# Kernel optimization log

Hardware: AMD Instinct MI355X
Metric: run time of the kernel (lower is better)

The kernel has to match this reference:

```python
import jax, jax.numpy as jnp
import numpy as np

WS = 7       # window size per spatial dim
SHIFT = 3    # cyclic shift = WS // 2
HEADS = 6


def _rel_pos_index():
    # [N, N] index into the (2*WS-1)^3 relative-position-bias table
    c = np.stack(np.meshgrid(np.arange(WS), np.arange(WS), np.arange(WS), indexing='ij')).reshape(3, -1)
    rel = (c[:, :, None] - c[:, None, :]).transpose(1, 2, 0) + (WS - 1)
    rel[:, :, 0] *= (2 * WS - 1) ** 2
    rel[:, :, 1] *= (2 * WS - 1)
    return rel.sum(-1)


def _attn_mask(D, H, W):
    # shifted-window attention mask: [nW, N, N] with 0 / -100
    img = np.zeros((D, H, W))
    sl = (slice(0, -WS), slice(-WS, -SHIFT), slice(-SHIFT, None))
    cnt = 0
    for d in sl:
        for h in sl:
            for w in sl:
                img[d, h, w] = cnt
                cnt += 1
    m = img.reshape(D // WS, WS, H // WS, WS, W // WS, WS).transpose(0, 2, 4, 1, 3, 5).reshape(-1, WS ** 3)
    return np.where(m[:, None, :] != m[:, :, None], -100.0, 0.0).astype(np.float32)


def _ln(x, g, b):
    mu = x.mean(-1, keepdims=True)
    var = ((x - mu) ** 2).mean(-1, keepdims=True)
    return (x - mu) * jax.lax.rsqrt(var + 1e-5) * g + b


def _win_part(x):
    B, D, H, W, C = x.shape
    x = x.reshape(B, D // WS, WS, H // WS, WS, W // WS, WS, C)
    return x.transpose(0, 1, 3, 5, 2, 4, 6, 7).reshape(B, -1, WS ** 3, C)


def _win_rev(xw, D, H, W):
    B, _, _, C = xw.shape
    x = xw.reshape(B, D // WS, H // WS, W // WS, WS, WS, WS, C)
    return x.transpose(0, 1, 4, 2, 5, 3, 6, 7).reshape(B, D, H, W, C)


def setup_inputs() -> dict:
    key = jax.random.key(0)
    ks = jax.random.split(key, 8)
    C, dff, Nh = 192, 768, HEADS
    s = 0.02
    return {
        'x': jax.random.normal(ks[0], (2, 28, 28, 28, C), jnp.float32),
        'ln1_g': jnp.ones((C,), jnp.float32),
        'ln1_b': jnp.zeros((C,), jnp.float32),
        'qkv_w': jax.random.normal(ks[1], (3 * C, C), jnp.float32) * s,
        'qkv_b': jnp.zeros((3 * C,), jnp.float32),
        'rpb': jax.random.normal(ks[2], ((2 * WS - 1) ** 3, Nh), jnp.float32) * s,
        'proj_w': jax.random.normal(ks[3], (C, C), jnp.float32) * s,
        'proj_b': jnp.zeros((C,), jnp.float32),
        'ln2_g': jnp.ones((C,), jnp.float32),
        'ln2_b': jnp.zeros((C,), jnp.float32),
        'fc1_w': jax.random.normal(ks[4], (dff, C), jnp.float32) * s,
        'fc1_b': jnp.zeros((dff,), jnp.float32),
        'fc2_w': jax.random.normal(ks[5], (C, dff), jnp.float32) * s,
        'fc2_b': jnp.zeros((C,), jnp.float32),
    }


def reference(x, ln1_g, ln1_b, qkv_w, qkv_b, rpb, proj_w, proj_b, ln2_g, ln2_b, fc1_w, fc1_b, fc2_w, fc2_b):
    B, D, H, W, C = x.shape
    hd = C // HEADS
    N = WS ** 3
    idx = jnp.asarray(_rel_pos_index())          # [N, N] int
    mask = jnp.asarray(_attn_mask(D, H, W))      # [nW, N, N]

    shortcut = x
    h = _ln(x, ln1_g, ln1_b)
    h = jnp.roll(h, (-SHIFT, -SHIFT, -SHIFT), axis=(1, 2, 3))
    xw = _win_part(h)                            # [B, nW, N, C]
    nW = xw.shape[1]

    qkv = xw @ qkv_w.T + qkv_b                   # [B, nW, N, 3C]
    qkv = qkv.reshape(B, nW, N, 3, HEADS, hd).transpose(3, 0, 1, 4, 2, 5)  # [3,B,nW,h,N,hd]
    q, k, v = qkv[0], qkv[1], qkv[2]

    scale = hd ** -0.5
    attn = jnp.einsum('bwhnd,bwhmd->bwhnm', q * scale, k)  # [B,nW,h,N,N]
    bias = rpb[idx].transpose(2, 0, 1)           # [h, N, N]
    attn = attn + bias + mask[None, :, None]
    attn = jax.nn.softmax(attn, axis=-1)

    o = jnp.einsum('bwhnm,bwhmd->bwhnd', attn, v)
    o = o.transpose(0, 1, 3, 2, 4).reshape(B, nW, N, C)
    o = o @ proj_w.T + proj_b
    o = _win_rev(o, D, H, W)
    o = jnp.roll(o, (SHIFT, SHIFT, SHIFT), axis=(1, 2, 3))

    x = shortcut + o
    h2 = _ln(x, ln2_g, ln2_b)
    h2 = jax.nn.gelu(h2 @ fc1_w.T + fc1_b, approximate=False)
    return x + (h2 @ fc2_w.T + fc2_b)
```

## Files before the change

### kernel.cpp

```cpp
#include <hip/hip_runtime.h>
#include <hip/hip_bf16.h>
#include <math.h>

typedef __hip_bfloat16 bf16;
typedef unsigned short u16;
typedef __attribute__((ext_vector_type(8))) short bf16x8;
typedef __attribute__((ext_vector_type(4))) short bf16x4;
typedef __attribute__((ext_vector_type(4))) float f32x4;

__device__ __forceinline__ float us2f(u16 u) { return __uint_as_float(((unsigned)u) << 16); }
__device__ __forceinline__ u16 f2us(float f) { bf16 h = __float2bfloat16(f); return *(u16*)&h; }

__device__ __forceinline__ float wave_bcast_sum(float v) {
#pragma unroll
    for (int off = 32; off > 0; off >>= 1) v += __shfl_down(v, off);
    return __shfl(v, 0);
}

__device__ __forceinline__ void glds16(const u16* g, u16* l) {
    __builtin_amdgcn_global_load_lds((const __attribute__((address_space(1))) void*)g,
                                     (__attribute__((address_space(3))) void*)l, 16, 0, 0);
}

__global__ __launch_bounds__(256) void k_f2b(const float* __restrict__ in, u16* __restrict__ out, int n) {
    int i = blockIdx.x * 256 + threadIdx.x;
    if (i < n) out[i] = f2us(in[i]);
}

__global__ __launch_bounds__(256) void k_bias(const float* __restrict__ rpb, float* __restrict__ bt) {
    int idx = blockIdx.x * 256 + threadIdx.x;
    if (idx >= 6 * 343 * 352) return;
    int h = idx / (343 * 352);
    int r = idx - h * (343 * 352);
    int n = r / 352, m = r - n * 352;
    float v = 0.0f;
    if (m < 343) {
        int ni = n / 49, nr = n - ni * 49, nj = nr / 7, nk = nr - nj * 7;
        int mi = m / 49, mr = m - mi * 49, mj = mr / 7, mk = mr - mj * 7;
        int d = (ni - mi) * 169 + (nj - mj) * 13 + (nk - mk) + 1098;
        v = rpb[d * 6 + h] * 1.4426950408889634f;
    }
    bt[idx] = v;
}

__global__ __launch_bounds__(256) void k_ln1_winpart(
    const float* __restrict__ x, const float* __restrict__ g, const float* __restrict__ b,
    u16* __restrict__ out)
{
    int lane = threadIdx.x & 63;
    int t = blockIdx.x * 4 + (threadIdx.x >> 6);
    int bidx = t / (64 * 343);
    int r = t - bidx * (64 * 343);
    int w = r / 343;
    int n = r - w * 343;
    int wd = w >> 4, wh = (w >> 2) & 3, ww = w & 3;
    int i = n / 49, rem = n - i * 49;
    int j = rem / 7, k = rem - j * 7;
    int sd = wd * 7 + i + 3; if (sd >= 28) sd -= 28;
    int sh = wh * 7 + j + 3; if (sh >= 28) sh -= 28;
    int sw = ww * 7 + k + 3; if (sw >= 28) sw -= 28;
    size_t src = ((((size_t)bidx * 28 + sd) * 28 + sh) * 28 + sw) * 192;
    float v0 = x[src + lane], v1 = x[src + lane + 64], v2 = x[src + lane + 128];
    float s  = wave_bcast_sum(v0 + v1 + v2);
    float mu = s * (1.0f / 192.0f);
    float s2 = wave_bcast_sum(v0 * v0 + v1 * v1 + v2 * v2);
    float rs = rsqrtf(s2 * (1.0f / 192.0f) - mu * mu + 1e-5f);
    u16* op = out + (size_t)t * 192;
    op[lane]       = f2us((v0 - mu) * rs * g[lane]       + b[lane]);
    op[lane + 64]  = f2us((v1 - mu) * rs * g[lane + 64]  + b[lane + 64]);
    op[lane + 128] = f2us((v2 - mu) * rs * g[lane + 128] + b[lane + 128]);
}

__global__ __launch_bounds__(256) void k_add_winrev_ln2(
    const float* __restrict__ x, const u16* __restrict__ projw,
    const float* __restrict__ g, const float* __restrict__ b,
    float* __restrict__ x1, u16* __restrict__ h2)
{
    int lane = threadIdx.x & 63;
    int t = blockIdx.x * 4 + (threadIdx.x >> 6);
    int sw_ = t % 28, t1 = t / 28;
    int sh_ = t1 % 28, t2 = t1 / 28;
    int sd_ = t2 % 28, bidx = t2 / 28;
    int rd = sd_ + 25; if (rd >= 28) rd -= 28;
    int rh = sh_ + 25; if (rh >= 28) rh -= 28;
    int rw = sw_ + 25; if (rw >= 28) rw -= 28;
    int wd = rd / 7, i = rd - wd * 7;
    int wh = rh / 7, j = rh - wh * 7;
    int ww = rw / 7, k = rw - ww * 7;
    int w = (wd << 4) + (wh << 2) + ww;
    int n = (i * 7 + j) * 7 + k;
    size_t src = (((size_t)(bidx * 64 + w)) * 343 + n) * 192;
    const float* xp = x + (size_t)t * 192;
    float v0 = xp[lane]       + us2f(projw[src + lane]);
    float v1 = xp[lane + 64]  + us2f(projw[src + lane + 64]);
    float v2 = xp[lane + 128] + us2f(projw[src + lane + 128]);
    float* op = x1 + (size_t)t * 192;
    op[lane] = v0; op[lane + 64] = v1; op[lane + 128] = v2;
    float s  = wave_bcast_sum(v0 + v1 + v2);
    float mu = s * (1.0f / 192.0f);
    float s2 = wave_bcast_sum(v0 * v0 + v1 * v1 + v2 * v2);
    float rs = rsqrtf(s2 * (1.0f / 192.0f) - mu * mu + 1e-5f);
    u16* hp = h2 + (size_t)t * 192;
    hp[lane]       = f2us((v0 - mu) * rs * g[lane]       + b[lane]);
    hp[lane + 64]  = f2us((v1 - mu) * rs * g[lane + 64]  + b[lane + 64]);
    hp[lane + 128] = f2us((v2 - mu) * rs * g[lane + 128] + b[lane + 128]);
}

template<int ACT, int OUT>
__global__ __launch_bounds__(256) void k_gemm_mfma(
    const u16* __restrict__ A, const u16* __restrict__ W, const float* __restrict__ bias,
    u16* __restrict__ outB, float* __restrict__ outF, const float* __restrict__ resid,
    int M, int Nc, int K)
{
    __shared__ __align__(16) u16 As[128 * 32];
    __shared__ __align__(16) u16 Bs[64 * 32];
    int tid = threadIdx.x;
    int lane = tid & 63, wv = tid >> 6;
    int quad = lane >> 4, l16 = lane & 15;
    int m0 = blockIdx.y << 7, n0 = blockIdx.x << 6;

    f32x4 acc[2][4] = {};
    int rowA0 = tid >> 2;
    int rowA1 = rowA0 + 64;
    int koff = (tid & 3) << 3;

    const u16* gA0 = A + (size_t)(m0 + rowA0) * K + koff;
    const u16* gA1 = A + (size_t)(m0 + rowA1) * K + koff;
    const u16* gB0 = W + (size_t)(n0 + rowA0) * K + koff;
    u16* lA0 = &As[wv * 512];
    u16* lA1 = &As[2048 + wv * 512];
    u16* lB0 = &Bs[wv * 512];

    for (int k0 = 0; k0 < K; k0 += 32) {
        glds16(gA0 + k0, lA0);
        glds16(gA1 + k0, lA1);
        glds16(gB0 + k0, lB0);
        __syncthreads();
        bf16x8 af[2], bfr[4];
#pragma unroll
        for (int mt = 0; mt < 2; mt++)
            af[mt] = *(const bf16x8*)&As[(wv * 32 + mt * 16 + l16) * 32 + quad * 8];
#pragma unroll
        for (int nt = 0; nt < 4; nt++)
            bfr[nt] = *(const bf16x8*)&Bs[(nt * 16 + l16) * 32 + quad * 8];
#pragma unroll
        for (int mt = 0; mt < 2; mt++)
#pragma unroll
            for (int nt = 0; nt < 4; nt++)
                acc[mt][nt] = __builtin_amdgcn_mfma_f32_16x16x32_bf16(af[mt], bfr[nt], acc[mt][nt], 0, 0, 0);
        __syncthreads();
    }
#pragma unroll
    for (int mt = 0; mt < 2; mt++) {
#pragma unroll
        for (int nt = 0; nt < 4; nt++) {
#pragma unroll
            for (int r = 0; r < 4; r++) {
                int m = m0 + wv * 32 + mt * 16 + quad * 4 + r;
                int n = n0 + nt * 16 + l16;
                float v = acc[mt][nt][r] + bias[n];
                if (ACT == 1) v = 0.5f * v * (1.0f + erff(v * 0.70710678118654752f));
                size_t off = (size_t)m * Nc + n;
                if (OUT == 1) outB[off] = f2us(v);
                else outF[off] = resid[off] + v;
            }
        }
    }
}

__global__ __launch_bounds__(256) void k_attn(
    const u16* __restrict__ qkv, const float* __restrict__ biasT, u16* __restrict__ o_win)
{
    int head = blockIdx.x;
    int w = blockIdx.y;
    int bidx = blockIdx.z;
    __shared__ __align__(16) u16 Ks[352 * 36];
    __shared__ __align__(16) u16 Vt[32 * 352];
    __shared__ __align__(16) u16 Pb[4][16 * 36];
    __shared__ unsigned char lab[352];
    int tid = threadIdx.x;
    int lane = tid & 63, wv = tid >> 6;
    int quad = lane >> 4, l16 = lane & 15;
    size_t base = ((size_t)(bidx * 64 + w)) * 343;

    for (int i = tid; i < 2816; i += 256) {
        int m = i >> 3;
        int d4 = (i & 7) << 2;
        ushort4 kv = {0, 0, 0, 0}, vv = {0, 0, 0, 0};
        if (m < 343) {
            size_t off = (base + m) * 576 + head * 32 + d4;
            kv = *(const ushort4*)(qkv + off + 192);
            vv = *(const ushort4*)(qkv + off + 384);
        }
        *(ushort4*)&Ks[m * 36 + d4] = kv;
        Vt[(d4 + 0) * 352 + m] = vv.x;
        Vt[(d4 + 1) * 352 + m] = vv.y;
        Vt[(d4 + 2) * 352 + m] = vv.z;
        Vt[(d4 + 3) * 352 + m] = vv.w;
    }
    int wd = w >> 4, wh = (w >> 2) & 3, ww = w & 3;
    for (int n = tid; n < 352; n += 256) {
        unsigned char lv = 255;
        if (n < 343) {
            int i = n / 49, rem = n - i * 49;
            int j = rem / 7, k = rem - j * 7;
            int gd = wd * 7 + i, gh = wh * 7 + j, gw = ww * 7 + k;
            int ld_ = (gd < 21) ? 0 : ((gd < 25) ? 1 : 2);
            int lh_ = (gh < 21) ? 0 : ((gh < 25) ? 1 : 2);
            int lw_ = (gw < 21) ? 0 : ((gw < 25) ? 1 : 2);
            lv = (unsigned char)(ld_ * 9 + lh_ * 3 + lw_);
        }
        lab[n] = lv;
    }
    __syncthreads();

    const float SL = 0.17677669529663687f * 1.4426950408889634f;
    u16* pbw = &Pb[wv][0];
    const f32x4 zero = {0.0f, 0.0f, 0.0f, 0.0f};

    for (int rt = wv; rt < 22; rt += 4) {
        int na = rt * 16 + l16; if (na > 342) na = 342;
        bf16x8 af = *(const bf16x8*)(qkv + (base + na) * 576 + head * 32 + quad * 8);
        int lr[4]; const float* bp[4];
#pragma unroll
        for (int r = 0; r < 4; r++) {
            int n = rt * 16 + quad * 4 + r; if (n > 342) n = 342;
            lr[r] = lab[n];
            bp[r] = biasT + ((size_t)(head * 343 + n)) * 352;
        }
        f32x4 o0 = zero, o1 = zero;
        float psum[4] = {0.0f, 0.0f, 0.0f, 0.0f};
        for (int c = 0; c < 11; c++) {
            int m0i = c * 32 + l16;
            int m1i = m0i + 16;
            float b0[4], b1[4];
#pragma unroll
            for (int r = 0; r < 4; r++) { b0[r] = bp[r][m0i]; b1[r] = bp[r][m1i]; }
            int lm0 = lab[m0i], lm1 = lab[m1i];
            const u16* kr0 = &Ks[m0i * 36 + quad * 8];
            const u16* kr1 = &Ks[m1i * 36 + quad * 8];
            bf16x4 k0a = *(const bf16x4*)kr0, k0b = *(const bf16x4*)(kr0 + 4);
            bf16x4 k1a = *(const bf16x4*)kr1, k1b = *(const bf16x4*)(kr1 + 4);
            bf16x8 kb0 = __builtin_shufflevector(k0a, k0b, 0, 1, 2, 3, 4, 5, 6, 7);
            bf16x8 kb1 = __builtin_shufflevector(k1a, k1b, 0, 1, 2, 3, 4, 5, 6, 7);
            f32x4 s0 = __builtin_amdgcn_mfma_f32_16x16x32_bf16(af, kb0, zero, 0, 0, 0);
            f32x4 s1 = __builtin_amdgcn_mfma_f32_16x16x32_bf16(af, kb1, zero, 0, 0, 0);
#pragma unroll
            for (int r = 0; r < 4; r++) {
                float p0 = exp2f(fmaf(s0[r], SL, b0[r]));
                p0 = (lm0 == lr[r]) ? p0 : 0.0f;
                psum[r] += p0;
                pbw[(quad * 4 + r) * 36 + l16] = f2us(p0);
                float p1 = exp2f(fmaf(s1[r], SL, b1[r]));
                p1 = (lm1 == lr[r]) ? p1 : 0.0f;
                psum[r] += p1;
                pbw[(quad * 4 + r) * 36 + 16 + l16] = f2us(p1);
            }
            asm volatile("s_waitcnt lgkmcnt(0)" ::: "memory");
            const u16* pr = &pbw[l16 * 36 + quad * 8];
            bf16x4 pa0 = *(const bf16x4*)pr, pa1 = *(const bf16x4*)(pr + 4);
            bf16x8 pa = __builtin_shufflevector(pa0, pa1, 0, 1, 2, 3, 4, 5, 6, 7);
            bf16x8 vb0 = *(const bf16x8*)&Vt[l16 * 352 + c * 32 + quad * 8];
            bf16x8 vb1 = *(const bf16x8*)&Vt[(16 + l16) * 352 + c * 32 + quad * 8];
            o0 = __builtin_amdgcn_mfma_f32_16x16x32_bf16(pa, vb0, o0, 0, 0, 0);
            o1 = __builtin_amdgcn_mfma_f32_16x16x32_bf16(pa, vb1, o1, 0, 0, 0);
        }
#pragma unroll
        for (int r = 0; r < 4; r++) {
#pragma unroll
            for (int off = 1; off < 16; off <<= 1)
                psum[r] += __shfl_xor(psum[r], off);
        }
#pragma unroll
        for (int r = 0; r < 4; r++) {
            int n = rt * 16 + quad * 4 + r;
            if (n < 343) {
                float inv = 1.0f / psum[r];
                u16* op = o_win + (base + n) * 192 + head * 32;
                op[l16]      = f2us(o0[r] * inv);
                op[l16 + 16] = f2us(o1[r] * inv);
            }
        }
    }
}

extern "C" void kernel_launch(void* const* d_in, const int* in_sizes, int n_in,
                              void* d_out, int out_size, void* d_ws, size_t ws_size,
                              hipStream_t stream)
{
    const float* x      = (const float*)d_in[0];
    const float* ln1_g  = (const float*)d_in[1];
    const float* ln1_b  = (const float*)d_in[2];
    const float* qkv_w  = (const float*)d_in[3];
    const float* qkv_b  = (const float*)d_in[4];
    const float* rpb    = (const float*)d_in[5];
    const float* proj_w = (const float*)d_in[6];
    const float* proj_b = (const float*)d_in[7];
    const float* ln2_g  = (const float*)d_in[8];
    const float* ln2_b  = (const float*)d_in[9];
    const float* fc1_w  = (const float*)d_in[10];
    const float* fc1_b  = (const float*)d_in[11];
    const float* fc2_w  = (const float*)d_in[12];
    const float* fc2_b  = (const float*)d_in[13];

    const int M = 43904;
    const size_t MC  = (size_t)M * 192;
    const size_t MC2 = MC * 2;

    char* ws = (char*)d_ws;
    u16* hA     = (u16*)ws;
    u16* qkvb   = (u16*)(ws + MC2);
    u16* projw  = (u16*)(ws + MC2);
    u16* gbuf   = (u16*)(ws + MC2);
    u16* fc1_wb = (u16*)(ws + 51u * 1024 * 1024);
    u16* fc2_wb = (u16*)(ws + 51u * 1024 * 1024 + 294912);
    float* out  = (float*)d_out;
    u16* qkv_wb  = (u16*)d_out;
    u16* proj_wb = (u16*)d_out + 110592;
    float* biasT = (float*)((char*)d_out + 4u * 1024 * 1024);

    k_f2b<<<432, 256, 0, stream>>>(qkv_w, qkv_wb, 110592);
    k_f2b<<<144, 256, 0, stream>>>(proj_w, proj_wb, 36864);
    k_bias<<<2830, 256, 0, stream>>>(rpb, biasT);
    k_ln1_winpart<<<M / 4, 256, 0, stream>>>(x, ln1_g, ln1_b, hA);
    k_gemm_mfma<0, 1><<<dim3(9, 343), 256, 0, stream>>>(hA, qkv_wb, qkv_b, qkvb, nullptr, nullptr, M, 576, 192);
    k_attn<<<dim3(6, 64, 2), 256, 0, stream>>>(qkvb, biasT, hA);
    k_f2b<<<576, 256, 0, stream>>>(fc1_w, fc1_wb, 147456);
    k_f2b<<<576, 256, 0, stream>>>(fc2_w, fc2_wb, 147456);
    k_gemm_mfma<0, 1><<<dim3(3, 343), 256, 0, stream>>>(hA, proj_wb, proj_b, projw, nullptr, nullptr, M, 192, 192);
    k_add_winrev_ln2<<<M / 4, 256, 0, stream>>>(x, projw, ln2_g, ln2_b, out, hA);
    const int CH0 = 22016, CH1 = 21888;
    k_gemm_mfma<1, 1><<<dim3(12, 172), 256, 0, stream>>>(hA, fc1_wb, fc1_b, gbuf, nullptr, nullptr, CH0, 768, 192);
    k_gemm_mfma<0, 2><<<dim3(3, 172), 256, 0, stream>>>(gbuf, fc2_wb, fc2_b, nullptr, out, out, CH0, 192, 768);
    k_gemm_mfma<1, 1><<<dim3(12, 171), 256, 0, stream>>>(hA + (size_t)CH0 * 192, fc1_wb, fc1_b, gbuf, nullptr, nullptr, CH1, 768, 192);
    k_gemm_mfma<0, 2><<<dim3(3, 171), 256, 0, stream>>>(gbuf, fc2_wb, fc2_b, nullptr, out + (size_t)CH0 * 192, out + (size_t)CH0 * 192, CH1, 192, 768);
}
```

Measured before the change: 340.9 us.

## Rewrite window attention with 32x32 MFMA transposed scores and register-resident P

The attention kernel switches from 16x16x32 to 32x32x16 MFMA tiles. It computes S transposed (keys by queries), so the probabilities can be repacked in registers with v_permlane32_swap and fed straight into the PV MFMA, which removes the per-wave LDS staging buffer for P and its wait. To support this, the bias table is stored transposed and padded to 352x352, and the LDS strides are changed. Separately, the GEMM gains double-buffered LDS so the next K-slice's global-to-LDS load overlaps the current MFMAs. The cost is more LDS in the GEMM and strided bias reads in attention.

```diff
diff --git a/kernel.cpp b/kernel.cpp
--- a/kernel.cpp
+++ b/kernel.cpp
@@ -5,8 +5,9 @@
 typedef __hip_bfloat16 bf16;
 typedef unsigned short u16;
 typedef __attribute__((ext_vector_type(8))) short bf16x8;
-typedef __attribute__((ext_vector_type(4))) short bf16x4;
 typedef __attribute__((ext_vector_type(4))) float f32x4;
+typedef __attribute__((ext_vector_type(16))) float f32x16;
+typedef __attribute__((ext_vector_type(4))) unsigned u32x4;
 
 __device__ __forceinline__ float us2f(u16 u) { return __uint_as_float(((unsigned)u) << 16); }
 __device__ __forceinline__ u16 f2us(float f) { bf16 h = __float2bfloat16(f); return *(u16*)&h; }
@@ -29,12 +30,12 @@
 
 __global__ __launch_bounds__(256) void k_bias(const float* __restrict__ rpb, float* __restrict__ bt) {
     int idx = blockIdx.x * 256 + threadIdx.x;
-    if (idx >= 6 * 343 * 352) return;
-    int h = idx / (343 * 352);
-    int r = idx - h * (343 * 352);
-    int n = r / 352, m = r - n * 352;
+    if (idx >= 6 * 352 * 352) return;
+    int h = idx / (352 * 352);
+    int r = idx - h * (352 * 352);
+    int m = r / 352, n = r - m * 352;
     float v = 0.0f;
-    if (m < 343) {
+    if (m < 343 && n < 343) {
         int ni = n / 49, nr = n - ni * 49, nj = nr / 7, nk = nr - nj * 7;
         int mi = m / 49, mr = m - mi * 49, mj = mr / 7, mk = mr - mj * 7;
         int d = (ni - mi) * 169 + (nj - mj) * 13 + (nk - mk) + 1098;
@@ -112,8 +113,8 @@
     u16* __restrict__ outB, float* __restrict__ outF, const float* __restrict__ resid,
     int M, int Nc, int K)
 {
-    __shared__ __align__(16) u16 As[128 * 32];
-    __shared__ __align__(16) u16 Bs[64 * 32];
+    __shared__ __align__(16) u16 As[2][128 * 32];
+    __shared__ __align__(16) u16 Bs[2][64 * 32];
     int tid = threadIdx.x;
     int lane = tid & 63, wv = tid >> 6;
     int quad = lane >> 4, l16 = lane & 15;
@@ -127,38 +128,47 @@
     const u16* gA0 = A + (size_t)(m0 + rowA0) * K + koff;
     const u16* gA1 = A + (size_t)(m0 + rowA1) * K + koff;
     const u16* gB0 = W + (size_t)(n0 + rowA0) * K + koff;
-    u16* lA0 = &As[wv * 512];
-    u16* lA1 = &As[2048 + wv * 512];
-    u16* lB0 = &Bs[wv * 512];
-
-    for (int k0 = 0; k0 < K; k0 += 32) {
-        glds16(gA0 + k0, lA0);
-        glds16(gA1 + k0, lA1);
-        glds16(gB0 + k0, lB0);
-        __syncthreads();
+
+    int nt = K >> 5;
+    glds16(gA0, &As[0][wv * 512]);
+    glds16(gA1, &As[0][2048 + wv * 512]);
+    glds16(gB0, &Bs[0][wv * 512]);
+    asm volatile("s_waitcnt vmcnt(0)" ::: "memory");
+    __builtin_amdgcn_s_barrier();
+
+    int cur = 0;
+    for (int t = 0; t < nt; ++t) {
+        if (t + 1 < nt) {
+            int k1 = (t + 1) << 5;
+            glds16(gA0 + k1, &As[cur ^ 1][wv * 512]);
+            glds16(gA1 + k1, &As[cur ^ 1][2048 + wv * 512]);
+            glds16(gB0 + k1, &Bs[cur ^ 1][wv * 512]);
+        }
         bf16x8 af[2], bfr[4];
 #pragma unroll
         for (int mt = 0; mt < 2; mt++)
-            af[mt] = *(const bf16x8*)&As[(wv * 32 + mt * 16 + l16) * 32 + quad * 8];
-#pragma unroll
-        for (int nt = 0; nt < 4; nt++)
-            bfr[nt] = *(const bf16x8*)&Bs[(nt * 16 + l16) * 32 + quad * 8];
+            af[mt] = *(const bf16x8*)&As[cur][(wv * 32 + mt * 16 + l16) * 32 + quad * 8];
+#pragma unroll
+        for (int nt2 = 0; nt2 < 4; nt2++)
+            bfr[nt2] = *(const bf16x8*)&Bs[cur][(nt2 * 16 + l16) * 32 + quad * 8];
 #pragma unroll
         for (int mt = 0; mt < 2; mt++)
 #pragma unroll
-            for (int nt = 0; nt < 4; nt++)
-                acc[mt][nt] = __builtin_amdgcn_mfma_f32_16x16x32_bf16(af[mt], bfr[nt], acc[mt][nt], 0, 0, 0);
-        __syncthreads();
+            for (int nt2 = 0; nt2 < 4; nt2++)
+                acc[mt][nt2] = __builtin_amdgcn_mfma_f32_16x16x32_bf16(af[mt], bfr[nt2], acc[mt][nt2], 0, 0, 0);
+        asm volatile("s_waitcnt vmcnt(0)" ::: "memory");
+        __builtin_amdgcn_s_barrier();
+        cur ^= 1;
     }
 #pragma unroll
     for (int mt = 0; mt < 2; mt++) {
 #pragma unroll
-        for (int nt = 0; nt < 4; nt++) {
+        for (int nt2 = 0; nt2 < 4; nt2++) {
 #pragma unroll
             for (int r = 0; r < 4; r++) {
                 int m = m0 + wv * 32 + mt * 16 + quad * 4 + r;
-                int n = n0 + nt * 16 + l16;
-                float v = acc[mt][nt][r] + bias[n];
+                int n = n0 + nt2 * 16 + l16;
+                float v = acc[mt][nt2][r] + bias[n];
                 if (ACT == 1) v = 0.5f * v * (1.0f + erff(v * 0.70710678118654752f));
                 size_t off = (size_t)m * Nc + n;
                 if (OUT == 1) outB[off] = f2us(v);
@@ -174,13 +184,13 @@
     int head = blockIdx.x;
     int w = blockIdx.y;
     int bidx = blockIdx.z;
-    __shared__ __align__(16) u16 Ks[352 * 36];
-    __shared__ __align__(16) u16 Vt[32 * 352];
-    __shared__ __align__(16) u16 Pb[4][16 * 36];
+    __shared__ __align__(16) u16 Ks[352 * 40];
+    __shared__ __align__(16) u16 Vt[32 * 360];
+    __shared__ float invs[4][32];
     __shared__ unsigned char lab[352];
     int tid = threadIdx.x;
     int lane = tid & 63, wv = tid >> 6;
-    int quad = lane >> 4, l16 = lane & 15;
+    int hi = lane >> 5, l31 = lane & 31;
     size_t base = ((size_t)(bidx * 64 + w)) * 343;
 
     for (int i = tid; i < 2816; i += 256) {
@@ -192,11 +202,11 @@
             kv = *(const ushort4*)(qkv + off + 192);
             vv = *(const ushort4*)(qkv + off + 384);
         }
-        *(ushort4*)&Ks[m * 36 + d4] = kv;
-        Vt[(d4 + 0) * 352 + m] = vv.x;
-        Vt[(d4 + 1) * 352 + m] = vv.y;
-        Vt[(d4 + 2) * 352 + m] = vv.z;
-        Vt[(d4 + 3) * 352 + m] = vv.w;
+        *(ushort4*)&Ks[m * 40 + d4] = kv;
+        Vt[(d4 + 0) * 360 + m] = vv.x;
+        Vt[(d4 + 1) * 360 + m] = vv.y;
+        Vt[(d4 + 2) * 360 + m] = vv.z;
+        Vt[(d4 + 3) * 360 + m] = vv.w;
     }
     int wd = w >> 4, wh = (w >> 2) & 3, ww = w & 3;
     for (int n = tid; n < 352; n += 256) {
@@ -215,70 +225,73 @@
     __syncthreads();
 
     const float SL = 0.17677669529663687f * 1.4426950408889634f;
-    u16* pbw = &Pb[wv][0];
-    const f32x4 zero = {0.0f, 0.0f, 0.0f, 0.0f};
-
-    for (int rt = wv; rt < 22; rt += 4) {
-        int na = rt * 16 + l16; if (na > 342) na = 342;
-        bf16x8 af = *(const bf16x8*)(qkv + (base + na) * 576 + head * 32 + quad * 8);
-        int lr[4]; const float* bp[4];
-#pragma unroll
-        for (int r = 0; r < 4; r++) {
-            int n = rt * 16 + quad * 4 + r; if (n > 342) n = 342;
-            lr[r] = lab[n];
-            bp[r] = biasT + ((size_t)(head * 343 + n)) * 352;
-        }
-        f32x4 o0 = zero, o1 = zero;
-        float psum[4] = {0.0f, 0.0f, 0.0f, 0.0f};
-        for (int c = 0; c < 11; c++) {
-            int m0i = c * 32 + l16;
-            int m1i = m0i + 16;
-            float b0[4], b1[4];
-#pragma unroll
-            for (int r = 0; r < 4; r++) { b0[r] = bp[r][m0i]; b1[r] = bp[r][m1i]; }
-            int lm0 = lab[m0i], lm1 = lab[m1i];
-            const u16* kr0 = &Ks[m0i * 36 + quad * 8];
-            const u16* kr1 = &Ks[m1i * 36 + quad * 8];
-            bf16x4 k0a = *(const bf16x4*)kr0, k0b = *(const bf16x4*)(kr0 + 4);
-            bf16x4 k1a = *(const bf16x4*)kr1, k1b = *(const bf16x4*)(kr1 + 4);
-            bf16x8 kb0 = __builtin_shufflevector(k0a, k0b, 0, 1, 2, 3, 4, 5, 6, 7);
-            bf16x8 kb1 = __builtin_shufflevector(k1a, k1b, 0, 1, 2, 3, 4, 5, 6, 7);
-            f32x4 s0 = __builtin_amdgcn_mfma_f32_16x16x32_bf16(af, kb0, zero, 0, 0, 0);
-            f32x4 s1 = __builtin_amdgcn_mfma_f32_16x16x32_bf16(af, kb1, zero, 0, 0, 0);
-#pragma unroll
-            for (int r = 0; r < 4; r++) {
-                float p0 = exp2f(fmaf(s0[r], SL, b0[r]));
-                p0 = (lm0 == lr[r]) ? p0 : 0.0f;
-                psum[r] += p0;
-                pbw[(quad * 4 + r) * 36 + l16] = f2us(p0);
-                float p1 = exp2f(fmaf(s1[r], SL, b1[r]));
-                p1 = (lm1 == lr[r]) ? p1 : 0.0f;
-                psum[r] += p1;
-                pbw[(quad * 4 + r) * 36 + 16 + l16] = f2us(p1);
+    const f32x16 z16 = {0,0,0,0,0,0,0,0,0,0,0,0,0,0,0,0};
+
+    for (int tile = wv; tile < 11; tile += 4) {
+        int n0 = tile * 32;
+        int nq = n0 + l31; if (nq > 342) nq = 342;
+        const u16* qp = qkv + (base + nq) * 576 + head * 32;
+        bf16x8 bq0 = *(const bf16x8*)(qp + hi * 8);
+        bf16x8 bq1 = *(const bf16x8*)(qp + 16 + hi * 8);
+        unsigned lr = lab[n0 + l31];
+        const float* bq = biasT + (size_t)head * 352 * 352 + n0 + l31;
+
+        f32x16 o = z16;
+        float psum = 0.0f;
+        for (int c = 0; c < 11; ++c) {
+            int mb = c * 32;
+            const u16* kp = &Ks[(mb + l31) * 40 + hi * 8];
+            bf16x8 ka0 = *(const bf16x8*)kp;
+            bf16x8 ka1 = *(const bf16x8*)(kp + 16);
+            f32x16 s = __builtin_amdgcn_mfma_f32_32x32x16_bf16(ka0, bq0, z16, 0, 0, 0);
+            s = __builtin_amdgcn_mfma_f32_32x32x16_bf16(ka1, bq1, s, 0, 0, 0);
+            unsigned labw[4];
+#pragma unroll
+            for (int g = 0; g < 4; ++g)
+                labw[g] = *(const unsigned*)&lab[mb + hi * 4 + g * 8];
+            float p[16];
+#pragma unroll
+            for (int r = 0; r < 16; ++r) {
+                int g = r >> 2, q = r & 3;
+                float bb = bq[(size_t)(mb + 4 * hi + 8 * g + q) * 352];
+                float e = exp2f(fmaf(s[r], SL, bb));
+                p[r] = (((labw[g] >> (8 * q)) & 255u) == lr) ? e : 0.0f;
+                psum += p[r];
             }
-            asm volatile("s_waitcnt lgkmcnt(0)" ::: "memory");
-            const u16* pr = &pbw[l16 * 36 + quad * 8];
-            bf16x4 pa0 = *(const bf16x4*)pr, pa1 = *(const bf16x4*)(pr + 4);
-            bf16x8 pa = __builtin_shufflevector(pa0, pa1, 0, 1, 2, 3, 4, 5, 6, 7);
-            bf16x8 vb0 = *(const bf16x8*)&Vt[l16 * 352 + c * 32 + quad * 8];
-            bf16x8 vb1 = *(const bf16x8*)&Vt[(16 + l16) * 352 + c * 32 + quad * 8];
-            o0 = __builtin_amdgcn_mfma_f32_16x16x32_bf16(pa, vb0, o0, 0, 0, 0);
-            o1 = __builtin_amdgcn_mfma_f32_16x16x32_bf16(pa, vb1, o1, 0, 0, 0);
-        }
-#pragma unroll
-        for (int r = 0; r < 4; r++) {
-#pragma unroll
-            for (int off = 1; off < 16; off <<= 1)
-                psum[r] += __shfl_xor(psum[r], off);
-        }
-#pragma unroll
-        for (int r = 0; r < 4; r++) {
-            int n = rt * 16 + quad * 4 + r;
+            unsigned pk0 = (unsigned)f2us(p[0])  | ((unsigned)f2us(p[1])  << 16);
+            unsigned pk1 = (unsigned)f2us(p[2])  | ((unsigned)f2us(p[3])  << 16);
+            unsigned pk2 = (unsigned)f2us(p[4])  | ((unsigned)f2us(p[5])  << 16);
+            unsigned pk3 = (unsigned)f2us(p[6])  | ((unsigned)f2us(p[7])  << 16);
+            unsigned pk4 = (unsigned)f2us(p[8])  | ((unsigned)f2us(p[9])  << 16);
+            unsigned pk5 = (unsigned)f2us(p[10]) | ((unsigned)f2us(p[11]) << 16);
+            unsigned pk6 = (unsigned)f2us(p[12]) | ((unsigned)f2us(p[13]) << 16);
+            unsigned pk7 = (unsigned)f2us(p[14]) | ((unsigned)f2us(p[15]) << 16);
+            asm volatile("v_permlane32_swap_b32 %0, %1" : "+v"(pk0), "+v"(pk2));
+            asm volatile("v_permlane32_swap_b32 %0, %1" : "+v"(pk1), "+v"(pk3));
+            asm volatile("v_permlane32_swap_b32 %0, %1" : "+v"(pk4), "+v"(pk6));
+            asm volatile("v_permlane32_swap_b32 %0, %1" : "+v"(pk5), "+v"(pk7));
+            u32x4 A1 = {pk0, pk1, pk2, pk3};
+            u32x4 A2 = {pk4, pk5, pk6, pk7};
+            bf16x8 pa0 = __builtin_bit_cast(bf16x8, A1);
+            bf16x8 pa1 = __builtin_bit_cast(bf16x8, A2);
+            const u16* vp = &Vt[l31 * 360 + mb + hi * 8];
+            bf16x8 vb0 = *(const bf16x8*)vp;
+            bf16x8 vb1 = *(const bf16x8*)(vp + 16);
+            o = __builtin_amdgcn_mfma_f32_32x32x16_bf16(pa0, vb0, o, 0, 0, 0);
+            o = __builtin_amdgcn_mfma_f32_32x32x16_bf16(pa1, vb1, o, 0, 0, 0);
+        }
+        psum += __shfl_xor(psum, 32);
+        float inv = 1.0f / psum;
+        invs[wv][l31] = inv;
+        asm volatile("s_waitcnt lgkmcnt(0)" ::: "memory");
+        __builtin_amdgcn_sched_barrier(0);
+#pragma unroll
+        for (int r = 0; r < 16; ++r) {
+            int crow = (r & 3) + 8 * (r >> 2) + 4 * hi;
+            int n = n0 + crow;
             if (n < 343) {
-                float inv = 1.0f / psum[r];
                 u16* op = o_win + (base + n) * 192 + head * 32;
-                op[l16]      = f2us(o0[r] * inv);
-                op[l16 + 16] = f2us(o1[r] * inv);
+                op[l31] = f2us(o[r] * invs[wv][crow]);
             }
         }
     }
@@ -321,7 +334,7 @@
 
     k_f2b<<<432, 256, 0, stream>>>(qkv_w, qkv_wb, 110592);
     k_f2b<<<144, 256, 0, stream>>>(proj_w, proj_wb, 36864);
-    k_bias<<<2830, 256, 0, stream>>>(rpb, biasT);
+    k_bias<<<2904, 256, 0, stream>>>(rpb, biasT);
     k_ln1_winpart<<<M / 4, 256, 0, stream>>>(x, ln1_g, ln1_b, hA);
     k_gemm_mfma<0, 1><<<dim3(9, 343), 256, 0, stream>>>(hA, qkv_wb, qkv_b, qkvb, nullptr, nullptr, M, 576, 192);
     k_attn<<<dim3(6, 64, 2), 256, 0, stream>>>(qkvb, biasT, hA);
```

After: 341.3 us. Within noise of the previous version (+0.1%).
